# Performance work log

Measured on AMD Instinct MI355X. Metric: run time of the kernel, lower is better.

The kernel has to match this reference:

```python
import jax, jax.numpy as jnp
import numpy as np

B, L, C, H, W, R = 1, 8, 16, 240, 480, 8
MID = C // 2          # HamiltonianGenerator mid channels
SE_MID = max(C // 16, 4)

SOBEL_X = jnp.array([[-1., 0., 1.], [-2., 0., 2.], [-1., 0., 1.]], jnp.float32).reshape(1, 1, 3, 3)
SOBEL_Y = jnp.array([[-1., -2., -1.], [0., 0., 0.], [1., 2., 1.]], jnp.float32).reshape(1, 1, 3, 3)


def _conv2d(x, w, b=None, padding='SAME'):
    y = jax.lax.conv_general_dilated(x, w, (1, 1), padding,
                                     dimension_numbers=('NCHW', 'OIHW', 'NCHW'))
    return y if b is None else y + b[None, :, None, None]


def _flow_field(x, w1, b1, w2, b2):
    # x: [B,L,C,H,W] -> flow [B,L,2,H,W] (HamiltonianGenerator)
    b_, l_, c_, h_, w_ = x.shape
    xf = x.reshape(b_ * l_, c_, h_, w_)
    f = jax.nn.silu(_conv2d(xf, w1, b1))
    f = _conv2d(f, w2, b2)                      # [N,2,H,W]
    phi, psi = f[:, :1], f[:, 1:]

    def grads(p):
        p = jnp.pad(p, ((0, 0), (0, 0), (0, 0), (1, 1)), mode='wrap')   # circular in W
        p = jnp.pad(p, ((0, 0), (0, 0), (1, 1), (0, 0)), mode='edge')   # replicate in H
        return (_conv2d(p, SOBEL_X, padding='VALID'),
                _conv2d(p, SOBEL_Y, padding='VALID'))

    gx_phi, gy_phi = grads(phi)
    gx_psi, gy_psi = grads(psi)
    lat = jnp.linspace(-np.pi / 2, np.pi / 2, h_).reshape(1, 1, h_, 1)
    metric = 1.0 / (jnp.cos(lat) + 1e-6)
    u = gx_phi * metric - gy_psi
    v = gy_phi + gx_psi * metric
    return jnp.tanh(jnp.concatenate([u, v], axis=1)).reshape(b_, l_, 2, h_, w_)


def _grid_sample_border(im, grid):
    # im: [C,H,W,R], grid: [H,W,2] in [-1,1]; bilinear, border pad, align_corners=False
    c_, h_, w_, r_ = im.shape
    xp = (grid[..., 0] + 1.0) * (w_ * 0.5) - 0.5
    yp = (grid[..., 1] + 1.0) * (h_ * 0.5) - 0.5
    xp = jnp.clip(xp, 0.0, w_ - 1.0)
    yp = jnp.clip(yp, 0.0, h_ - 1.0)
    x0f = jnp.floor(xp); y0f = jnp.floor(yp)
    wx = (xp - x0f)[None, :, :, None]
    wy = (yp - y0f)[None, :, :, None]
    x0 = x0f.astype(jnp.int32); y0 = y0f.astype(jnp.int32)
    x1 = jnp.minimum(x0 + 1, w_ - 1); y1 = jnp.minimum(y0 + 1, h_ - 1)
    v00 = im[:, y0, x0, :]; v01 = im[:, y0, x1, :]
    v10 = im[:, y1, x0, :]; v11 = im[:, y1, x1, :]
    top = v00 * (1 - wx) + v01 * wx
    bot = v10 * (1 - wx) + v11 * wx
    return top * (1 - wy) + bot * wy


def _forward(x, h0, listT, hw1, hb1, hw2, hb2, sw1, sb1, sw2, sb2):
    b_, l_, c_, h_, w_ = x.shape
    flow = _flow_field(x, hw1, hb1, hw2, hb2)           # [B,L,2,H,W]
    gy, gx = jnp.meshgrid(jnp.linspace(-1.0, 1.0, h_),
                          jnp.linspace(-1.0, 1.0, w_), indexing='ij')
    base_grid = jnp.stack([gx, gy], axis=-1)            # [H,W,2]
    sample = jax.vmap(_grid_sample_border, in_axes=(0, 0))

    def se_gate(xf):
        # LatitudeAwareSE on [B,C,H,W]: pool over W, MLP over C per latitude
        y = xf.mean(axis=-1)                                              # [B,C,H]
        y = jax.nn.silu(jnp.einsum('bch,mc->bmh', y, sw1) + sb1[None, :, None])
        y = jax.nn.sigmoid(jnp.einsum('bmh,cm->bch', y, sw2) + sb2[None, :, None])
        return xf * y[..., None]

    def step(h, inp):
        flow_t, dt_t, x_t = inp                          # [B,2,H,W], [B], [B,C,H,W]
        disp = flow_t * dt_t[:, None, None, None]
        grid = base_grid[None] - jnp.moveaxis(disp, 1, -1)   # [B,H,W,2]
        h = sample(h, grid)                              # LieTransport advection
        h = h + x_t[..., None]                           # inject current frame
        y = se_gate(h.mean(axis=-1))                     # readout over rank + SE gate
        return h, y

    xs = (jnp.moveaxis(flow, 1, 0), listT.T, jnp.moveaxis(x, 1, 0))
    _, ys = jax.lax.scan(step, h0, xs)                   # ys: [L,B,C,H,W]
    return jnp.moveaxis(ys, 0, 1)                        # [B,L,C,H,W]


def setup_inputs() -> dict:
    key = jax.random.key(0)
    ks = jax.random.split(key, 8)
    return {
        'x': jax.random.normal(ks[0], (B, L, C, H, W), jnp.float32),
        'h0': jax.random.normal(ks[1], (B, C, H, W, R), jnp.float32),
        'listT': jax.random.uniform(ks[2], (B, L), jnp.float32, 0.1, 1.0),
        'ham_w1': jax.random.normal(ks[3], (MID, C, 3, 3), jnp.float32) * 0.08,
        'ham_b1': jnp.zeros((MID,), jnp.float32),
        'ham_w2': jax.random.normal(ks[4], (2, MID, 3, 3), jnp.float32) * 0.08,
        'ham_b2': jnp.zeros((2,), jnp.float32),
        'se_w1': jax.random.normal(ks[5], (SE_MID, C), jnp.float32) * 0.25,
        'se_b1': jnp.zeros((SE_MID,), jnp.float32),
        'se_w2': jax.random.normal(ks[6], (C, SE_MID), jnp.float32) * 0.25,
        'se_b2': jnp.zeros((C,), jnp.float32),
    }


def reference(x, h0, listT, ham_w1, ham_b1, ham_w2, ham_b2, se_w1, se_b1, se_w2, se_b2):
    return _forward(x, h0, listT, ham_w1, ham_b1, ham_w2, ham_b2, se_w1, se_b1, se_w2, se_b2)
```

## Files before the change

kernel.cpp:

```cpp
#include <hip/hip_runtime.h>
#include <math.h>

constexpr int Lq = 8, Cq = 16, Hq = 240, Wq = 480, MIDq = 8, SEM = 4;
constexpr int HWq = Hq * Wq;
constexpr int CHUNK = 48;
constexpr int NCH = Wq / CHUNK;

__device__ __forceinline__ float sigmoidf_(float v) { return 1.0f / (1.0f + expf(-v)); }

__global__ void k_conv1(const float* __restrict__ x, const float* __restrict__ w1,
                        const float* __restrict__ b1, float* __restrict__ f1) {
    int b = blockIdx.x;
    int l = b & 7, y = b >> 3;
    int t = threadIdx.x;
    if (t >= Wq / 4) return;
    int xi = t * 4;
    float acc[MIDq][4];
#pragma unroll
    for (int m = 0; m < MIDq; m++) {
        float bv = b1[m];
#pragma unroll
        for (int o = 0; o < 4; o++) acc[m][o] = bv;
    }
#pragma unroll 1
    for (int ic = 0; ic < Cq; ic++) {
        const float* xin = x + (size_t)(l * Cq + ic) * HWq;
        const float* wrow = w1 + ic * 9;
#pragma unroll
        for (int r = 0; r < 3; r++) {
            int yy = y + r - 1;
            if (yy < 0 || yy >= Hq) continue;
            const float* rp = xin + yy * Wq;
            float4 mid = *(const float4*)(rp + xi);
            float lft = (xi > 0) ? rp[xi - 1] : 0.f;
            float rgt = (xi + 4 < Wq) ? rp[xi + 4] : 0.f;
            float in6[6] = {lft, mid.x, mid.y, mid.z, mid.w, rgt};
#pragma unroll
            for (int m = 0; m < MIDq; m++) {
                const float* wp = wrow + m * (Cq * 9) + r * 3;
                float w0 = wp[0], w1v = wp[1], w2 = wp[2];
#pragma unroll
                for (int o = 0; o < 4; o++)
                    acc[m][o] = fmaf(w0, in6[o],
                                fmaf(w1v, in6[o + 1],
                                fmaf(w2, in6[o + 2], acc[m][o])));
            }
        }
    }
    size_t rowoff = (size_t)y * Wq + xi;
#pragma unroll
    for (int m = 0; m < MIDq; m++) {
        float4 v;
        float a0 = acc[m][0], a1 = acc[m][1], a2 = acc[m][2], a3 = acc[m][3];
        v.x = a0 * sigmoidf_(a0);
        v.y = a1 * sigmoidf_(a1);
        v.z = a2 * sigmoidf_(a2);
        v.w = a3 * sigmoidf_(a3);
        *(float4*)(f1 + (size_t)(l * MIDq + m) * HWq + rowoff) = v;
    }
}

__global__ void k_conv2(const float* __restrict__ f1, const float* __restrict__ w2,
                        const float* __restrict__ b2, float* __restrict__ f) {
    int b = blockIdx.x;
    int l = b & 7, y = b >> 3;
    int t = threadIdx.x;
    if (t >= Wq / 4) return;
    int xi = t * 4;
    float acc[2][4];
#pragma unroll
    for (int m = 0; m < 2; m++) {
        float bv = b2[m];
#pragma unroll
        for (int o = 0; o < 4; o++) acc[m][o] = bv;
    }
#pragma unroll 1
    for (int ic = 0; ic < MIDq; ic++) {
        const float* fin = f1 + (size_t)(l * MIDq + ic) * HWq;
        const float* wrow = w2 + ic * 9;
#pragma unroll
        for (int r = 0; r < 3; r++) {
            int yy = y + r - 1;
            if (yy < 0 || yy >= Hq) continue;
            const float* rp = fin + yy * Wq;
            float4 mid = *(const float4*)(rp + xi);
            float lft = (xi > 0) ? rp[xi - 1] : 0.f;
            float rgt = (xi + 4 < Wq) ? rp[xi + 4] : 0.f;
            float in6[6] = {lft, mid.x, mid.y, mid.z, mid.w, rgt};
#pragma unroll
            for (int m = 0; m < 2; m++) {
                const float* wp = wrow + m * (MIDq * 9) + r * 3;
                float w0 = wp[0], w1v = wp[1], w2v = wp[2];
#pragma unroll
                for (int o = 0; o < 4; o++)
                    acc[m][o] = fmaf(w0, in6[o],
                                fmaf(w1v, in6[o + 1],
                                fmaf(w2v, in6[o + 2], acc[m][o])));
            }
        }
    }
    size_t rowoff = (size_t)y * Wq + xi;
#pragma unroll
    for (int m = 0; m < 2; m++) {
        float4 v = {acc[m][0], acc[m][1], acc[m][2], acc[m][3]};
        *(float4*)(f + (size_t)(l * 2 + m) * HWq + rowoff) = v;
    }
}

__global__ void k_flow(const float* __restrict__ f, float* __restrict__ flow) {
    int idx = blockIdx.x * blockDim.x + threadIdx.x;
    if (idx >= Lq * HWq) return;
    int l = idx / HWq, rem = idx % HWq, y = rem / Wq, x = rem % Wq;
    const float* phi = f + (size_t)(l * 2 + 0) * HWq;
    const float* psi = f + (size_t)(l * 2 + 1) * HWq;
    float ph[3][3], ps[3][3];
#pragma unroll
    for (int i = 0; i < 3; i++) {
        int yy = y + i - 1;
        yy = yy < 0 ? 0 : (yy >= Hq ? Hq - 1 : yy);
#pragma unroll
        for (int j = 0; j < 3; j++) {
            int xx = x + j - 1;
            xx = (xx + Wq) % Wq;
            ph[i][j] = phi[yy * Wq + xx];
            ps[i][j] = psi[yy * Wq + xx];
        }
    }
    float gxp = (ph[0][2] - ph[0][0]) + 2.f * (ph[1][2] - ph[1][0]) + (ph[2][2] - ph[2][0]);
    float gyp = (ph[2][0] + 2.f * ph[2][1] + ph[2][2]) - (ph[0][0] + 2.f * ph[0][1] + ph[0][2]);
    float gxs = (ps[0][2] - ps[0][0]) + 2.f * (ps[1][2] - ps[1][0]) + (ps[2][2] - ps[2][0]);
    float gys = (ps[2][0] + 2.f * ps[2][1] + ps[2][2]) - (ps[0][0] + 2.f * ps[0][1] + ps[0][2]);
    float latf = (float)(-M_PI * 0.5 + (double)y * (M_PI / (double)(Hq - 1)));
    float metric = (float)(1.0 / (cos((double)latf) + 1e-6));
    float u = gxp * metric - gys;
    float v = gyp + gxs * metric;
    flow[(size_t)(l * 2 + 0) * HWq + rem] = tanhf(u);
    flow[(size_t)(l * 2 + 1) * HWq + rem] = tanhf(v);
}

__global__ void k_m0(const float* __restrict__ h0, float* __restrict__ m0) {
    int px = blockIdx.x * 256 + threadIdx.x;
    const float4* h4 = (const float4*)h0;
    float4* mp = (float4*)(m0 + (size_t)px * Cq);
#pragma unroll
    for (int cq = 0; cq < 4; cq++) {
        float vals[4];
#pragma unroll
        for (int cc = 0; cc < 4; cc++) {
            int c = cq * 4 + cc;
            float4 a = h4[(size_t)(c * HWq + px) * 2];
            float4 b = h4[(size_t)(c * HWq + px) * 2 + 1];
            vals[cc] = (a.x + a.y + a.z + a.w + b.x + b.y + b.z + b.w) * 0.125f;
        }
        float4 o = {vals[0], vals[1], vals[2], vals[3]};
        mp[cq] = o;
    }
}

__global__ __launch_bounds__(192) void k_warp(const float* __restrict__ min_,
                       float* __restrict__ mout, const float* __restrict__ flow_l,
                       const float* __restrict__ xl, const float* __restrict__ listT,
                       int l, float* __restrict__ rows_part) {
    int b = blockIdx.x;
    int row = b / NCH;
    int chunk = b - row * NCH;
    int xbase = chunk * CHUNK;
    int t = threadIdx.x;
    int pxl = t >> 2, csub = t & 3;

    __shared__ float sx[Cq][CHUNK + 1];
    const float* xrowbase = xl + (size_t)row * Wq + xbase;
#pragma unroll
    for (int it = 0; it < 4; it++) {
        int fidx = it * 192 + t;
        int c = fidx / CHUNK;
        int p = fidx - c * CHUNK;
        sx[c][p] = xrowbase[(size_t)c * HWq + p];
    }
    __syncthreads();

    int x = xbase + pxl;
    float dt = listT[l];
    float u = flow_l[row * Wq + x];
    float v = flow_l[HWq + row * Wq + x];
    float gx = (x * (2.0f / (Wq - 1)) - 1.0f) - u * dt;
    float gy = (row * (2.0f / (Hq - 1)) - 1.0f) - v * dt;
    float xp = fminf(fmaxf((gx + 1.0f) * (Wq * 0.5f) - 0.5f, 0.0f), (float)(Wq - 1));
    float yp = fminf(fmaxf((gy + 1.0f) * (Hq * 0.5f) - 0.5f, 0.0f), (float)(Hq - 1));
    float x0f = floorf(xp), y0f = floorf(yp);
    float wx = xp - x0f, wy = yp - y0f;
    int x0 = (int)x0f, y0 = (int)y0f;
    int x1 = min(x0 + 1, Wq - 1), y1 = min(y0 + 1, Hq - 1);

    const float4* m4 = (const float4*)min_;
    float4 A = m4[(size_t)(y0 * Wq + x0) * 4 + csub];
    float4 B = m4[(size_t)(y0 * Wq + x1) * 4 + csub];
    float4 C = m4[(size_t)(y1 * Wq + x0) * 4 + csub];
    float4 D = m4[(size_t)(y1 * Wq + x1) * 4 + csub];
    float w00 = (1.f - wx) * (1.f - wy), w01 = wx * (1.f - wy);
    float w10 = (1.f - wx) * wy, w11 = wx * wy;
    int c0 = csub * 4;
    float r0 = w00 * A.x + w01 * B.x + w10 * C.x + w11 * D.x + sx[c0 + 0][pxl];
    float r1 = w00 * A.y + w01 * B.y + w10 * C.y + w11 * D.y + sx[c0 + 1][pxl];
    float r2 = w00 * A.z + w01 * B.z + w10 * C.z + w11 * D.z + sx[c0 + 2][pxl];
    float r3 = w00 * A.w + w01 * B.w + w10 * C.w + w11 * D.w + sx[c0 + 3][pxl];

    float4 o = {r0, r1, r2, r3};
    ((float4*)(mout + (size_t)(row * Wq + x) * Cq))[csub] = o;

    __shared__ float lred[Cq][CHUNK + 1];
    lred[c0 + 0][pxl] = r0;
    lred[c0 + 1][pxl] = r1;
    lred[c0 + 2][pxl] = r2;
    lred[c0 + 3][pxl] = r3;
    __syncthreads();
    if (t < Cq) {
        float s = 0.f;
#pragma unroll
        for (int k = 0; k < CHUNK; k++) s += lred[t][k];
        rows_part[(size_t)b * Cq + t] = s;
    }
}

__global__ __launch_bounds__(192) void k_out(const float* __restrict__ m,
                       const float* __restrict__ rows_part,
                       const float* __restrict__ sw1, const float* __restrict__ sb1,
                       const float* __restrict__ sw2, const float* __restrict__ sb2,
                       float* __restrict__ out_l) {
    int b = blockIdx.x;
    int row = b / NCH;
    int chunk = b - row * NCH;
    int xbase = chunk * CHUNK;
    int t = threadIdx.x;
    int pxl = t >> 2, csub = t & 3;

    __shared__ float lm[CHUNK][Cq + 1];
    float4 vv = ((const float4*)(m + (size_t)(row * Wq + xbase + pxl) * Cq))[csub];
    lm[pxl][csub * 4 + 0] = vv.x;
    lm[pxl][csub * 4 + 1] = vv.y;
    lm[pxl][csub * 4 + 2] = vv.z;
    lm[pxl][csub * 4 + 3] = vv.w;

    __shared__ float ym[Cq];
    __shared__ float zz[SEM];
    __shared__ float gates[Cq];
    if (t < Cq) {
        float s = 0.f;
#pragma unroll
        for (int k = 0; k < NCH; k++) s += rows_part[(size_t)(row * NCH + k) * Cq + t];
        ym[t] = s * (1.0f / Wq);
    }
    __syncthreads();
    if (t < SEM) {
        float a = sb1[t];
#pragma unroll
        for (int i = 0; i < Cq; i++) a = fmaf(sw1[t * Cq + i], ym[i], a);
        zz[t] = a * sigmoidf_(a);
    }
    __syncthreads();
    if (t < Cq) {
        float a = sb2[t];
#pragma unroll
        for (int mm = 0; mm < SEM; mm++) a = fmaf(sw2[t * SEM + mm], zz[mm], a);
        gates[t] = sigmoidf_(a);
    }
    __syncthreads();

    int c = t / 12;
    int g = t - c * 12;
    float gv = gates[c];
    float4 o;
    o.x = lm[g * 4 + 0][c] * gv;
    o.y = lm[g * 4 + 1][c] * gv;
    o.z = lm[g * 4 + 2][c] * gv;
    o.w = lm[g * 4 + 3][c] * gv;
    *(float4*)(out_l + (size_t)c * HWq + row * Wq + xbase + g * 4) = o;
}

extern "C" void kernel_launch(void* const* d_in, const int* in_sizes, int n_in,
                              void* d_out, int out_size, void* d_ws, size_t ws_size,
                              hipStream_t stream) {
    const float* x = (const float*)d_in[0];
    const float* h0 = (const float*)d_in[1];
    const float* listT = (const float*)d_in[2];
    const float* hw1 = (const float*)d_in[3];
    const float* hb1 = (const float*)d_in[4];
    const float* hw2 = (const float*)d_in[5];
    const float* hb2 = (const float*)d_in[6];
    const float* sw1 = (const float*)d_in[7];
    const float* sb1 = (const float*)d_in[8];
    const float* sw2 = (const float*)d_in[9];
    const float* sb2 = (const float*)d_in[10];
    float* out = (float*)d_out;
    char* ws = (char*)d_ws;

    size_t off = 0;
    float* flow = (float*)(ws + off); off += sizeof(float) * (size_t)Lq * 2 * HWq;
    float* f    = (float*)(ws + off); off += sizeof(float) * (size_t)Lq * 2 * HWq;
    float* f1   = (float*)(ws + off); off += sizeof(float) * (size_t)Lq * MIDq * HWq;
    float* mA   = (float*)(ws + off); off += sizeof(float) * (size_t)HWq * Cq;
    float* mB   = (float*)(ws + off); off += sizeof(float) * (size_t)HWq * Cq;
    float* rp   = (float*)(ws + off); off += sizeof(float) * (size_t)(HWq / CHUNK) * Cq;

    k_conv1<<<Lq * Hq, 128, 0, stream>>>(x, hw1, hb1, f1);
    k_conv2<<<Lq * Hq, 128, 0, stream>>>(f1, hw2, hb2, f);
    k_flow<<<(Lq * HWq + 255) / 256, 256, 0, stream>>>(f, flow);
    k_m0<<<HWq / 256, 256, 0, stream>>>(h0, mA);

    float* bufs[2] = {mA, mB};
    for (int l = 0; l < Lq; l++) {
        float* min_ = bufs[l & 1];
        float* mout = bufs[(l + 1) & 1];
        k_warp<<<HWq / CHUNK, 192, 0, stream>>>(min_, mout, flow + (size_t)l * 2 * HWq,
                                                x + (size_t)l * Cq * HWq, listT, l, rp);
        k_out<<<HWq / CHUNK, 192, 0, stream>>>(mout, rp, sw1, sb1, sw2, sb2,
                                               out + (size_t)l * Cq * HWq);
    }
}
```

Before: 187.9 us.

## Fuse warp and SE-gating kernels into one row-per-block step kernel

Replaces the per-step pair of kernels (warp with partial row sums, then SE gating) with a single kernel where each 1024-thread block handles a whole image row. The row's channel sums are reduced in shared memory and wavefront shuffles, so the rows_part buffer, the second launch and the reread of m are removed. The trade is only 240 blocks per step with large shared memory, which can reduce occupancy and latency hiding. The conv loops also get unroll 2.

```diff
diff --git a/kernel.cpp b/kernel.cpp
--- a/kernel.cpp
+++ b/kernel.cpp
@@ -3,8 +3,6 @@
 
 constexpr int Lq = 8, Cq = 16, Hq = 240, Wq = 480, MIDq = 8, SEM = 4;
 constexpr int HWq = Hq * Wq;
-constexpr int CHUNK = 48;
-constexpr int NCH = Wq / CHUNK;
 
 __device__ __forceinline__ float sigmoidf_(float v) { return 1.0f / (1.0f + expf(-v)); }
 
@@ -22,7 +20,7 @@
 #pragma unroll
         for (int o = 0; o < 4; o++) acc[m][o] = bv;
     }
-#pragma unroll 1
+#pragma unroll 2
     for (int ic = 0; ic < Cq; ic++) {
         const float* xin = x + (size_t)(l * Cq + ic) * HWq;
         const float* wrow = w1 + ic * 9;
@@ -74,7 +72,7 @@
 #pragma unroll
         for (int o = 0; o < 4; o++) acc[m][o] = bv;
     }
-#pragma unroll 1
+#pragma unroll 2
     for (int ic = 0; ic < MIDq; ic++) {
         const float* fin = f1 + (size_t)(l * MIDq + ic) * HWq;
         const float* wrow = w2 + ic * 9;
@@ -157,124 +155,106 @@
     }
 }
 
-__global__ __launch_bounds__(192) void k_warp(const float* __restrict__ min_,
+__global__ __launch_bounds__(1024) void k_step(const float* __restrict__ min_,
                        float* __restrict__ mout, const float* __restrict__ flow_l,
                        const float* __restrict__ xl, const float* __restrict__ listT,
-                       int l, float* __restrict__ rows_part) {
-    int b = blockIdx.x;
-    int row = b / NCH;
-    int chunk = b - row * NCH;
-    int xbase = chunk * CHUNK;
-    int t = threadIdx.x;
-    int pxl = t >> 2, csub = t & 3;
-
-    __shared__ float sx[Cq][CHUNK + 1];
-    const float* xrowbase = xl + (size_t)row * Wq + xbase;
-#pragma unroll
-    for (int it = 0; it < 4; it++) {
-        int fidx = it * 192 + t;
-        int c = fidx / CHUNK;
-        int p = fidx - c * CHUNK;
-        sx[c][p] = xrowbase[(size_t)c * HWq + p];
-    }
-    __syncthreads();
-
-    int x = xbase + pxl;
-    float dt = listT[l];
-    float u = flow_l[row * Wq + x];
-    float v = flow_l[HWq + row * Wq + x];
-    float gx = (x * (2.0f / (Wq - 1)) - 1.0f) - u * dt;
-    float gy = (row * (2.0f / (Hq - 1)) - 1.0f) - v * dt;
-    float xp = fminf(fmaxf((gx + 1.0f) * (Wq * 0.5f) - 0.5f, 0.0f), (float)(Wq - 1));
-    float yp = fminf(fmaxf((gy + 1.0f) * (Hq * 0.5f) - 0.5f, 0.0f), (float)(Hq - 1));
-    float x0f = floorf(xp), y0f = floorf(yp);
-    float wx = xp - x0f, wy = yp - y0f;
-    int x0 = (int)x0f, y0 = (int)y0f;
-    int x1 = min(x0 + 1, Wq - 1), y1 = min(y0 + 1, Hq - 1);
-
-    const float4* m4 = (const float4*)min_;
-    float4 A = m4[(size_t)(y0 * Wq + x0) * 4 + csub];
-    float4 B = m4[(size_t)(y0 * Wq + x1) * 4 + csub];
-    float4 C = m4[(size_t)(y1 * Wq + x0) * 4 + csub];
-    float4 D = m4[(size_t)(y1 * Wq + x1) * 4 + csub];
-    float w00 = (1.f - wx) * (1.f - wy), w01 = wx * (1.f - wy);
-    float w10 = (1.f - wx) * wy, w11 = wx * wy;
-    int c0 = csub * 4;
-    float r0 = w00 * A.x + w01 * B.x + w10 * C.x + w11 * D.x + sx[c0 + 0][pxl];
-    float r1 = w00 * A.y + w01 * B.y + w10 * C.y + w11 * D.y + sx[c0 + 1][pxl];
-    float r2 = w00 * A.z + w01 * B.z + w10 * C.z + w11 * D.z + sx[c0 + 2][pxl];
-    float r3 = w00 * A.w + w01 * B.w + w10 * C.w + w11 * D.w + sx[c0 + 3][pxl];
-
-    float4 o = {r0, r1, r2, r3};
-    ((float4*)(mout + (size_t)(row * Wq + x) * Cq))[csub] = o;
-
-    __shared__ float lred[Cq][CHUNK + 1];
-    lred[c0 + 0][pxl] = r0;
-    lred[c0 + 1][pxl] = r1;
-    lred[c0 + 2][pxl] = r2;
-    lred[c0 + 3][pxl] = r3;
-    __syncthreads();
-    if (t < Cq) {
-        float s = 0.f;
-#pragma unroll
-        for (int k = 0; k < CHUNK; k++) s += lred[t][k];
-        rows_part[(size_t)b * Cq + t] = s;
-    }
-}
-
-__global__ __launch_bounds__(192) void k_out(const float* __restrict__ m,
-                       const float* __restrict__ rows_part,
+                       int l,
                        const float* __restrict__ sw1, const float* __restrict__ sb1,
                        const float* __restrict__ sw2, const float* __restrict__ sb2,
                        float* __restrict__ out_l) {
-    int b = blockIdx.x;
-    int row = b / NCH;
-    int chunk = b - row * NCH;
-    int xbase = chunk * CHUNK;
+    constexpr int STR = 17;
+    __shared__ float sm[Wq * STR];
+    __shared__ float csum[Cq];
+    __shared__ float zl[SEM];
+    __shared__ float gl[Cq];
+
+    int y = blockIdx.x;
     int t = threadIdx.x;
-    int pxl = t >> 2, csub = t & 3;
-
-    __shared__ float lm[CHUNK][Cq + 1];
-    float4 vv = ((const float4*)(m + (size_t)(row * Wq + xbase + pxl) * Cq))[csub];
-    lm[pxl][csub * 4 + 0] = vv.x;
-    lm[pxl][csub * 4 + 1] = vv.y;
-    lm[pxl][csub * 4 + 2] = vv.z;
-    lm[pxl][csub * 4 + 3] = vv.w;
-
-    __shared__ float ym[Cq];
-    __shared__ float zz[SEM];
-    __shared__ float gates[Cq];
-    if (t < Cq) {
+    int wave = t >> 6, lane = t & 63;
+    bool act = t < 2 * Wq;
+    int px = act ? (t >> 1) : (Wq - 1);
+    int half = t & 1;
+    int c0 = half * 8;
+
+    float dt = listT[l];
+    float mn[8];
+    {
+        float u = flow_l[y * Wq + px];
+        float v = flow_l[HWq + y * Wq + px];
+        float gx = (px * (2.0f / (Wq - 1)) - 1.0f) - u * dt;
+        float gy = (y * (2.0f / (Hq - 1)) - 1.0f) - v * dt;
+        float xp = fminf(fmaxf((gx + 1.0f) * (Wq * 0.5f) - 0.5f, 0.0f), (float)(Wq - 1));
+        float yp = fminf(fmaxf((gy + 1.0f) * (Hq * 0.5f) - 0.5f, 0.0f), (float)(Hq - 1));
+        float x0f = floorf(xp), y0f = floorf(yp);
+        float wx = xp - x0f, wy = yp - y0f;
+        int x0 = (int)x0f, y0 = (int)y0f;
+        int x1 = min(x0 + 1, Wq - 1), y1 = min(y0 + 1, Hq - 1);
+        const float4* m4 = (const float4*)min_;
+        size_t b00 = (size_t)(y0 * Wq + x0) * 4 + (half * 2);
+        size_t b01 = (size_t)(y0 * Wq + x1) * 4 + (half * 2);
+        size_t b10 = (size_t)(y1 * Wq + x0) * 4 + (half * 2);
+        size_t b11 = (size_t)(y1 * Wq + x1) * 4 + (half * 2);
+        float4 A0 = m4[b00], A1 = m4[b00 + 1];
+        float4 B0 = m4[b01], B1 = m4[b01 + 1];
+        float4 C0 = m4[b10], C1 = m4[b10 + 1];
+        float4 D0 = m4[b11], D1 = m4[b11 + 1];
+        float w00 = (1.f - wx) * (1.f - wy), w01 = wx * (1.f - wy);
+        float w10 = (1.f - wx) * wy, w11 = wx * wy;
+        const float* xb = xl + y * Wq + px;
+        float xv[8];
+#pragma unroll
+        for (int j = 0; j < 8; j++) xv[j] = xb[(size_t)(c0 + j) * HWq];
+        mn[0] = w00 * A0.x + w01 * B0.x + w10 * C0.x + w11 * D0.x + xv[0];
+        mn[1] = w00 * A0.y + w01 * B0.y + w10 * C0.y + w11 * D0.y + xv[1];
+        mn[2] = w00 * A0.z + w01 * B0.z + w10 * C0.z + w11 * D0.z + xv[2];
+        mn[3] = w00 * A0.w + w01 * B0.w + w10 * C0.w + w11 * D0.w + xv[3];
+        mn[4] = w00 * A1.x + w01 * B1.x + w10 * C1.x + w11 * D1.x + xv[4];
+        mn[5] = w00 * A1.y + w01 * B1.y + w10 * C1.y + w11 * D1.y + xv[5];
+        mn[6] = w00 * A1.z + w01 * B1.z + w10 * C1.z + w11 * D1.z + xv[6];
+        mn[7] = w00 * A1.w + w01 * B1.w + w10 * C1.w + w11 * D1.w + xv[7];
+    }
+    if (act) {
+        float4* mo = (float4*)(mout + (size_t)(y * Wq + px) * Cq + c0);
+        float4 o0 = {mn[0], mn[1], mn[2], mn[3]};
+        float4 o1 = {mn[4], mn[5], mn[6], mn[7]};
+        mo[0] = o0;
+        mo[1] = o1;
+#pragma unroll
+        for (int j = 0; j < 8; j++) sm[px * STR + c0 + j] = mn[j];
+    }
+    __syncthreads();
+    {
         float s = 0.f;
 #pragma unroll
-        for (int k = 0; k < NCH; k++) s += rows_part[(size_t)(row * NCH + k) * Cq + t];
-        ym[t] = s * (1.0f / Wq);
+        for (int k = 0; k < 8; k++) {
+            int p = k * 64 + lane;
+            if (p < Wq) s += sm[p * STR + wave];
+        }
+#pragma unroll
+        for (int off = 32; off > 0; off >>= 1) s += __shfl_down(s, off, 64);
+        if (lane == 0) csum[wave] = s;
     }
     __syncthreads();
     if (t < SEM) {
         float a = sb1[t];
 #pragma unroll
-        for (int i = 0; i < Cq; i++) a = fmaf(sw1[t * Cq + i], ym[i], a);
-        zz[t] = a * sigmoidf_(a);
+        for (int i = 0; i < Cq; i++) a = fmaf(sw1[t * Cq + i], csum[i] * (1.0f / Wq), a);
+        zl[t] = a * sigmoidf_(a);
     }
     __syncthreads();
     if (t < Cq) {
         float a = sb2[t];
 #pragma unroll
-        for (int mm = 0; mm < SEM; mm++) a = fmaf(sw2[t * SEM + mm], zz[mm], a);
-        gates[t] = sigmoidf_(a);
-    }
-    __syncthreads();
-
-    int c = t / 12;
-    int g = t - c * 12;
-    float gv = gates[c];
-    float4 o;
-    o.x = lm[g * 4 + 0][c] * gv;
-    o.y = lm[g * 4 + 1][c] * gv;
-    o.z = lm[g * 4 + 2][c] * gv;
-    o.w = lm[g * 4 + 3][c] * gv;
-    *(float4*)(out_l + (size_t)c * HWq + row * Wq + xbase + g * 4) = o;
+        for (int m = 0; m < SEM; m++) a = fmaf(sw2[t * SEM + m], zl[m], a);
+        gl[t] = sigmoidf_(a);
+    }
+    __syncthreads();
+    if (act) {
+        float* ob = out_l + y * Wq + px;
+#pragma unroll
+        for (int j = 0; j < 8; j++)
+            ob[(size_t)(c0 + j) * HWq] = mn[j] * gl[c0 + j];
+    }
 }
 
 extern "C" void kernel_launch(void* const* d_in, const int* in_sizes, int n_in,
@@ -300,7 +280,6 @@
     float* f1   = (float*)(ws + off); off += sizeof(float) * (size_t)Lq * MIDq * HWq;
     float* mA   = (float*)(ws + off); off += sizeof(float) * (size_t)HWq * Cq;
     float* mB   = (float*)(ws + off); off += sizeof(float) * (size_t)HWq * Cq;
-    float* rp   = (float*)(ws + off); off += sizeof(float) * (size_t)(HWq / CHUNK) * Cq;
 
     k_conv1<<<Lq * Hq, 128, 0, stream>>>(x, hw1, hb1, f1);
     k_conv2<<<Lq * Hq, 128, 0, stream>>>(f1, hw2, hb2, f);
@@ -311,9 +290,9 @@
     for (int l = 0; l < Lq; l++) {
         float* min_ = bufs[l & 1];
         float* mout = bufs[(l + 1) & 1];
-        k_warp<<<HWq / CHUNK, 192, 0, stream>>>(min_, mout, flow + (size_t)l * 2 * HWq,
-                                                x + (size_t)l * Cq * HWq, listT, l, rp);
-        k_out<<<HWq / CHUNK, 192, 0, stream>>>(mout, rp, sw1, sb1, sw2, sb2,
-                                               out + (size_t)l * Cq * HWq);
-    }
-}
+        k_step<<<Hq, 1024, 0, stream>>>(min_, mout, flow + (size_t)l * 2 * HWq,
+                                        x + (size_t)l * Cq * HWq, listT, l,
+                                        sw1, sb1, sw2, sb2,
+                                        out + (size_t)l * Cq * HWq);
+    }
+}
```

New measurement: 164.7 us. -12.3%, faster.
